# Performance work log

Measured on AMD Instinct MI355X. Metric: run time of the kernel, lower is better.

## Reference

```python
import jax, jax.numpy as jnp
import numpy as np

N = 50000
E = 600000
IN_DIM = 128
D = 32          # out_dim per head
H = 4           # heads
M = 3           # num metapaths
HID = 128       # semantic attention hidden
NEG_SLOPE = 0.2


def setup_inputs() -> dict:
    key = jax.random.key(0)
    ks = jax.random.split(key, 12)
    x = jax.random.normal(ks[0], (N, IN_DIM), dtype=jnp.float32)
    mp_edge_index = jax.random.randint(ks[1], (M, 2, E), 0, N, dtype=jnp.int64)
    s = 1.0 / np.sqrt(IN_DIM)
    W = jax.random.normal(ks[2], (M, IN_DIM, H * D), dtype=jnp.float32) * s
    att_src = jax.random.normal(ks[3], (M, H, D), dtype=jnp.float32) * (1.0 / np.sqrt(D))
    att_dst = jax.random.normal(ks[4], (M, H, D), dtype=jnp.float32) * (1.0 / np.sqrt(D))
    bias = jnp.zeros((M, H * D), dtype=jnp.float32)
    ln_gamma = jnp.ones((H * D,), dtype=jnp.float32)
    ln_beta = jnp.zeros((H * D,), dtype=jnp.float32)
    sem_W1 = jax.random.normal(ks[5], (H * D, HID), dtype=jnp.float32) * (1.0 / np.sqrt(H * D))
    sem_b1 = jnp.zeros((HID,), dtype=jnp.float32)
    sem_W2 = jax.random.normal(ks[6], (HID, 1), dtype=jnp.float32) * (1.0 / np.sqrt(HID))
    return dict(x=x, mp_edge_index=mp_edge_index, W=W, att_src=att_src,
                att_dst=att_dst, bias=bias, ln_gamma=ln_gamma, ln_beta=ln_beta,
                sem_W1=sem_W1, sem_b1=sem_b1, sem_W2=sem_W2)


def _gat_conv(x, edge_index, W_m, a_src, a_dst, b_m):
    # PyG GATConv (add_self_loops=True, concat=True). x: [N, F_in]
    n = x.shape[0]
    h = (x @ W_m).reshape(n, H, D)                       # [N, H, D]
    loops = jnp.arange(n, dtype=edge_index.dtype)
    src = jnp.concatenate([edge_index[0], loops])        # [E+N]
    dst = jnp.concatenate([edge_index[1], loops])
    alpha_s = jnp.einsum('nhd,hd->nh', h, a_src)         # [N, H]
    alpha_d = jnp.einsum('nhd,hd->nh', h, a_dst)
    e = jax.nn.leaky_relu(alpha_s[src] + alpha_d[dst], NEG_SLOPE)  # [E+N, H]
    # segment softmax over edges grouped by destination node
    e_max = jax.ops.segment_max(e, dst, num_segments=n)
    e = jnp.exp(e - e_max[dst])
    denom = jax.ops.segment_sum(e, dst, num_segments=n)
    alpha = e / (denom[dst] + 1e-16)                     # [E+N, H]
    msg = h[src] * alpha[:, :, None]                     # [E+N, H, D]
    out = jax.ops.segment_sum(msg, dst, num_segments=n)  # [N, H, D]
    return out.reshape(n, H * D) + b_m


def _layer_norm(y, gamma, beta):
    mu = y.mean(-1, keepdims=True)
    var = y.var(-1, keepdims=True)
    return (y - mu) * jax.lax.rsqrt(var + 1e-5) * gamma + beta


def reference(x, mp_edge_index, W, att_src, att_dst, bias, ln_gamma, ln_beta,
              sem_W1, sem_b1, sem_W2):
    embs = []
    for i in range(M):
        emb = _gat_conv(x, mp_edge_index[i], W[i], att_src[i], att_dst[i], bias[i])
        emb = jax.nn.elu(_layer_norm(emb, ln_gamma, ln_beta))
        embs.append(emb)
    z = jnp.stack(embs, axis=1)                          # [N, M, H*D]
    # semantic attention
    w = (jnp.tanh(z @ sem_W1 + sem_b1) @ sem_W2).mean(0)  # [M, 1]
    beta = jax.nn.softmax(w, axis=0)                      # [M, 1]
    out_emb = (beta[None, :, :] * z).sum(1)               # [N, H*D]
    att_mp = beta.squeeze()                               # [M]
    return out_emb, att_mp
```

## Files before the change

### kernel.cpp

```cpp
#include <hip/hip_runtime.h>
#include <hip/hip_bf16.h>

#define N_NODES 50000
#define N_EDGES 600000
#define NMETA   3
#define LTOT (NMETA * N_NODES)
#define SPAN_SHIFT 9
#define NBUCK 98
#define BCAP 8192
#define NCHUNK 147
#define NABLK 782
#define NSLOT (NMETA * NBUCK * BCAP)
#define NSEMBLK ((LTOT / 16 + 3) / 4)
#define LOG2E 1.4426950408889634f

typedef unsigned short u16;
typedef short bf16x8 __attribute__((ext_vector_type(8)));
typedef float f32x4 __attribute__((ext_vector_type(4)));

__device__ __forceinline__ float bf2f(u16 v) {
    union { unsigned int u; float f; } x; x.u = ((unsigned int)v) << 16; return x.f;
}
__device__ __forceinline__ float u2f(unsigned int u) {
    union { unsigned int u; float f; } x; x.u = u; return x.f;
}
__device__ __forceinline__ u16 f2bf(float f) {
    return __hip_bfloat16_raw(__float2bfloat16(f)).x;
}

#if __has_builtin(__builtin_amdgcn_fdot2_f32_bf16)
#define HAS_DOT2 1
typedef __bf16 bf16x2v __attribute__((ext_vector_type(2)));
__device__ __forceinline__ float dot2bf(unsigned hp, unsigned ep, float acc) {
    return __builtin_amdgcn_fdot2_f32_bf16(
        __builtin_bit_cast(bf16x2v, hp), __builtin_bit_cast(bf16x2v, ep), acc, false);
}
#else
#define HAS_DOT2 0
#endif

__global__ __launch_bounds__(256) void k_build1(
    const int* __restrict__ ei, int* __restrict__ gcnt,
    unsigned* __restrict__ pairs,
    const float* __restrict__ W, const float* __restrict__ W1,
    u16* __restrict__ WT, u16* __restrict__ W1T)
{
    const int bid = blockIdx.x;
    const int t = threadIdx.x;
    if (bid >= NMETA * NCHUNK) {
        int idx = (bid - NMETA * NCHUNK) * 256 + t;
        if (idx < NMETA * 16384) {
            int m = idx >> 14, r = idx & 16383;
            int col = r >> 7, k = r & 127;
            WT[idx] = f2bf(W[(m << 14) + k * 128 + col]);
        } else {
            int r = idx - NMETA * 16384;
            int col = r >> 7, k = r & 127;
            W1T[r] = f2bf(W1[k * 128 + col]);
        }
        return;
    }
    const int m = bid / NCHUNK;
    const int e0 = (bid % NCHUNK) * 4096;
    __shared__ int cnt[NBUCK];
    __shared__ int gbase[NBUCK];
    if (t < NBUCK) cnt[t] = 0;
    __syncthreads();
    const int* srcp = ei + (size_t)m * 2 * N_EDGES;
    const int* dstp = srcp + N_EDGES;
    int sa[16], da[16], sl[16];
    #pragma unroll
    for (int j = 0; j < 16; ++j) {
        int e = e0 + j * 256 + t;
        if (e < N_EDGES) {
            int s = srcp[e], d = dstp[e];
            if ((unsigned)s >= N_NODES) s = 0;
            if ((unsigned)d >= N_NODES) d = 0;
            sa[j] = s; da[j] = d;
            sl[j] = atomicAdd(&cnt[d >> SPAN_SHIFT], 1);
        } else sl[j] = -1;
    }
    __syncthreads();
    if (t < NBUCK) gbase[t] = atomicAdd(&gcnt[(m * NBUCK + t) * 16], cnt[t]);
    __syncthreads();
    #pragma unroll
    for (int j = 0; j < 16; ++j) {
        if (sl[j] < 0) continue;
        int b = da[j] >> SPAN_SHIFT;
        int pos = gbase[b] + sl[j];
        if (pos < BCAP)
            pairs[(size_t)(m * NBUCK + b) * BCAP + pos] =
                ((unsigned)(da[j] & 511) << 23) | (unsigned)(sa[j] * 128);
    }
}

__global__ __launch_bounds__(256) void k_build2(
    const int* __restrict__ gcnt, const unsigned* __restrict__ pairs,
    int* __restrict__ row_start, int* __restrict__ row_end, int* __restrict__ eidx,
    int* __restrict__ ptot,
    const float* __restrict__ x, const u16* __restrict__ WT,
    const float* __restrict__ att_src, const float* __restrict__ att_dst,
    u16* __restrict__ h, float* __restrict__ alpha_s, float* __restrict__ alpha_d)
{
    const int bid = blockIdx.x;
    const int t = threadIdx.x;
    if (bid < NMETA * NBUCK) {
        const int m = bid / NBUCK, b = bid % NBUCK;
        __shared__ int cnt[512];
        __shared__ int off[512];
        __shared__ int wsum[4];
        int nb = gcnt[(m * NBUCK + b) * 16]; if (nb > BCAP) nb = BCAP;
        const int base = (m * NBUCK + b) * BCAP;
        cnt[t] = 0; cnt[t + 256] = 0;
        __syncthreads();
        for (int e = t; e < nb; e += 256) {
            int dl = (int)(pairs[(size_t)base + e] >> 23);
            atomicAdd(&cnt[dl], 1);
        }
        __syncthreads();
        int c0 = cnt[2 * t], c1 = cnt[2 * t + 1];
        int v0p = (c0 + 3) & ~3, v1p = (c1 + 3) & ~3;
        int s = v0p + v1p;
        int lane = t & 63, wv = t >> 6;
        int incl = s;
        #pragma unroll
        for (int o = 1; o < 64; o <<= 1) {
            int u = __shfl_up(incl, o);
            if (lane >= o) incl += u;
        }
        if (lane == 63) wsum[wv] = incl;
        __syncthreads();
        int woff = 0;
        for (int i = 0; i < wv; ++i) woff += wsum[i];
        int ex = woff + incl - s;
        off[2 * t] = ex;
        off[2 * t + 1] = ex + v0p;
        if (t == 255) {
            int tot = ex + v0p + v1p;
            ptot[m * NBUCK + b] = tot < BCAP ? tot : BCAP;
        }
        for (int q = ex + c0; q < ex + v0p && q < BCAP; ++q) eidx[base + q] = 0;
        for (int q = ex + v0p + c1; q < ex + v0p + v1p && q < BCAP; ++q) eidx[base + q] = 0;
        __syncthreads();
        const int node0 = b << SPAN_SHIFT;
        for (int i = t; i < 512; i += 256) {
            int n = node0 + i;
            if (n < N_NODES) {
                int st = base + off[i];
                row_start[m * N_NODES + n] = st;
                row_end[m * N_NODES + n]   = st + cnt[i];
            }
        }
        __syncthreads();
        for (int e = t; e < nb; e += 256) {
            unsigned pv = pairs[(size_t)base + e];
            int dl = (int)(pv >> 23);
            int pos = atomicAdd(&off[dl], 1);
            if (pos >= BCAP) continue;
            eidx[base + pos] = (int)pv;
        }
        return;
    }
    const int g = bid - NMETA * NBUCK;
    const int bx = g % NABLK, m = g / NABLK;
    const int wv = t >> 6, lane = t & 63;
    const int row0 = (bx * 4 + wv) * 16;
    if (row0 >= N_NODES) return;
    const int lhi = lane >> 4, llo = lane & 15;
    const float* xrow = x + (size_t)(row0 + llo) * 128 + lhi * 8;
    bf16x8 a[4];
    #pragma unroll
    for (int ks = 0; ks < 4; ++ks) {
        float4 f0 = *(const float4*)(xrow + ks * 32);
        float4 f1 = *(const float4*)(xrow + ks * 32 + 4);
        bf16x8 av;
        av[0] = f2bf(f0.x); av[1] = f2bf(f0.y); av[2] = f2bf(f0.z); av[3] = f2bf(f0.w);
        av[4] = f2bf(f1.x); av[5] = f2bf(f1.y); av[6] = f2bf(f1.z); av[7] = f2bf(f1.w);
        a[ks] = av;
    }
    const u16* wbase = WT + (size_t)m * 16384 + (size_t)llo * 128 + lhi * 8;
    u16* hm = h + ((size_t)m * N_NODES + row0) * 128;
    float sp[4][4], dp[4][4];
    #pragma unroll
    for (int i = 0; i < 4; ++i)
        #pragma unroll
        for (int r = 0; r < 4; ++r) { sp[i][r] = 0.f; dp[i][r] = 0.f; }
    #pragma unroll
    for (int cf = 0; cf < 8; ++cf) {
        f32x4 acc = {0.f, 0.f, 0.f, 0.f};
        const u16* wp = wbase + cf * 16 * 128;
        #pragma unroll
        for (int ks = 0; ks < 4; ++ks) {
            bf16x8 bb = *(const bf16x8*)(wp + ks * 32);
            acc = __builtin_amdgcn_mfma_f32_16x16x32_bf16(a[ks], bb, acc, 0, 0, 0);
        }
        const int col = cf * 16 + llo;
        const int hh = cf >> 1;
        const float as = att_src[m * 128 + col];
        const float adv = att_dst[m * 128 + col];
        #pragma unroll
        for (int r = 0; r < 4; ++r) {
            hm[(size_t)(lhi * 4 + r) * 128 + col] = f2bf(acc[r]);
            sp[hh][r] += acc[r] * as;
            dp[hh][r] += acc[r] * adv;
        }
    }
    #pragma unroll
    for (int o = 1; o <= 8; o <<= 1) {
        #pragma unroll
        for (int i = 0; i < 4; ++i)
            #pragma unroll
            for (int r = 0; r < 4; ++r) {
                sp[i][r] += __shfl_xor(sp[i][r], o);
                dp[i][r] += __shfl_xor(dp[i][r], o);
            }
    }
    if (llo == 0) {
        #pragma unroll
        for (int r = 0; r < 4; ++r) {
            int n = row0 + lhi * 4 + r;
            f32x4 vs = {sp[0][r] * LOG2E, sp[1][r] * LOG2E, sp[2][r] * LOG2E, sp[3][r] * LOG2E};
            f32x4 vd = {dp[0][r] * LOG2E, dp[1][r] * LOG2E, dp[2][r] * LOG2E, dp[3][r] * LOG2E};
            *(f32x4*)(alpha_s + ((size_t)m * N_NODES + n) * 4) = vs;
            *(f32x4*)(alpha_d + ((size_t)m * N_NODES + n) * 4) = vd;
        }
    }
}

__global__ __launch_bounds__(256) void k_ew(
    const int* __restrict__ ptot, int* __restrict__ eidx,
    const float* __restrict__ alpha_s, const float* __restrict__ alpha_d,
    u16* __restrict__ ew)
{
    for (int sidx = blockIdx.x * 256 + threadIdx.x; sidx < NSLOT; sidx += gridDim.x * 256) {
        const int bucket = sidx >> 13;
        const int i = sidx & (BCAP - 1);
        if (i >= ptot[bucket]) continue;
        const int m = bucket / NBUCK, b = bucket % NBUCK;
        const int node0 = b << SPAN_SHIFT;
        int v = eidx[sidx];
        int src128 = v & 0x7FFFFF;
        int dl = (unsigned)v >> 23;
        const float* as_m = alpha_s + (size_t)m * N_NODES * 4;
        const float* ad_m = alpha_d + (size_t)m * N_NODES * 4;
        f32x4 as4 = *(const f32x4*)(as_m + (src128 >> 5));
        f32x4 ad4 = *(const f32x4*)(ad_m + (size_t)(node0 + dl) * 4);
        u16* ewp = ew + (size_t)(sidx >> 2) * 16 + (sidx & 3);
        #pragma unroll
        for (int k = 0; k < 4; ++k) {
            float pre = as4[k] + ad4[k];
            pre = fmaxf(pre, 0.2f * pre);
            ewp[k * 4] = f2bf(exp2f(pre));
        }
        eidx[sidx] = src128 * 2;
    }
}

__global__ __launch_bounds__(256) void k_gather(
    const int* __restrict__ row_start, const int* __restrict__ row_end,
    const int* __restrict__ eidx, const u16* __restrict__ ew,
    const float* __restrict__ alpha_s, const float* __restrict__ alpha_d,
    const u16* __restrict__ h,
    const float* __restrict__ bias, const float* __restrict__ gamma,
    const float* __restrict__ lbeta,
    u16* __restrict__ z)
{
    long long w = ((long long)blockIdx.x * blockDim.x + threadIdx.x) >> 6;
    if (w >= (long long)LTOT) return;
    int m = (int)(w / N_NODES), n = (int)(w % N_NODES);
    int lane = threadIdx.x & 63, hh = lane >> 4;
    const char* h_m = (const char*)(h + (size_t)m * N_NODES * 128);
    const char* ewb = (const char*)ew;
    const int lb = lane * 4;
    const float* as_m = alpha_s + (size_t)m * N_NODES * 4;
    const float* ad_m = alpha_d + (size_t)m * N_NODES * 4;
    float pre = as_m[n * 4 + hh] + ad_m[n * 4 + hh];
    pre = fmaxf(pre, 0.2f * pre);
    float ev = exp2f(pre);
    float esum = ev;
    unsigned hv = *(const unsigned*)(h_m + (size_t)n * 256 + lb);
    float acc0 = ev * u2f(hv << 16), acc1 = ev * u2f(hv & 0xffff0000u);
    int p = row_start[m * N_NODES + n];
    const int end = row_end[m * N_NODES + n];
    for (; p + 3 < end; p += 4) {
        int4 o4 = *(const int4*)(eidx + p);
        uint2 ewv = *(const uint2*)(ewb + (size_t)(p + hh) * 8);
        unsigned h1 = *(const unsigned*)(h_m + o4.x + lb);
        unsigned h2 = *(const unsigned*)(h_m + o4.y + lb);
        unsigned h3 = *(const unsigned*)(h_m + o4.z + lb);
        unsigned h4 = *(const unsigned*)(h_m + o4.w + lb);
#if HAS_DOT2
        unsigned lo12 = __builtin_amdgcn_perm(h2, h1, 0x05040100u);
        unsigned hi12 = __builtin_amdgcn_perm(h2, h1, 0x07060302u);
        unsigned lo34 = __builtin_amdgcn_perm(h4, h3, 0x05040100u);
        unsigned hi34 = __builtin_amdgcn_perm(h4, h3, 0x07060302u);
        acc0 = dot2bf(lo12, ewv.x, acc0);
        acc1 = dot2bf(hi12, ewv.x, acc1);
        acc0 = dot2bf(lo34, ewv.y, acc0);
        acc1 = dot2bf(hi34, ewv.y, acc1);
        esum = dot2bf(0x3F803F80u, ewv.x, esum);
        esum = dot2bf(0x3F803F80u, ewv.y, esum);
#else
        float e1 = u2f(ewv.x << 16), e2 = u2f(ewv.x & 0xffff0000u);
        float e3 = u2f(ewv.y << 16), e4 = u2f(ewv.y & 0xffff0000u);
        esum += (e1 + e2) + (e3 + e4);
        acc0 += e1 * u2f(h1 << 16) + e2 * u2f(h2 << 16)
              + e3 * u2f(h3 << 16) + e4 * u2f(h4 << 16);
        acc1 += e1 * u2f(h1 & 0xffff0000u) + e2 * u2f(h2 & 0xffff0000u)
              + e3 * u2f(h3 & 0xffff0000u) + e4 * u2f(h4 & 0xffff0000u);
#endif
    }
    for (; p < end; ++p) {
        int o1 = eidx[p];
        float e1 = bf2f(*(const u16*)(ewb + (size_t)((p & ~3) + hh) * 8 + (p & 3) * 2));
        unsigned h1 = *(const unsigned*)(h_m + o1 + lb);
        esum += e1;
        acc0 += e1 * u2f(h1 << 16);
        acc1 += e1 * u2f(h1 & 0xffff0000u);
    }
    float rinv = 1.f / (esum + 1e-16f);
    float v0 = acc0 * rinv + bias[m * 128 + lane * 2];
    float v1 = acc1 * rinv + bias[m * 128 + lane * 2 + 1];
    float s1 = v0 + v1, s2 = v0 * v0 + v1 * v1;
    #pragma unroll
    for (int o = 32; o >= 1; o >>= 1) { s1 += __shfl_xor(s1, o); s2 += __shfl_xor(s2, o); }
    float mu = s1 * (1.f / 128.f);
    float var = s2 * (1.f / 128.f) - mu * mu;
    float rs = rsqrtf(var + 1e-5f);
    float o0 = (v0 - mu) * rs * gamma[lane * 2]     + lbeta[lane * 2];
    float o1 = (v1 - mu) * rs * gamma[lane * 2 + 1] + lbeta[lane * 2 + 1];
    o0 = o0 > 0.f ? o0 : (__expf(o0) - 1.f);
    o1 = o1 > 0.f ? o1 : (__expf(o1) - 1.f);
    ushort2 outv; outv.x = f2bf(o0); outv.y = f2bf(o1);
    *(ushort2*)(z + ((size_t)n * NMETA + m) * 128 + lane * 2) = outv;
}

__global__ __launch_bounds__(256) void k_sem(
    const u16* __restrict__ z, const u16* __restrict__ W1T,
    const float* __restrict__ b1, const float* __restrict__ W2,
    float4* __restrict__ partial)
{
    __shared__ float part[NMETA];
    const int t = threadIdx.x;
    if (t < NMETA) part[t] = 0.f;
    __syncthreads();
    const int wv = t >> 6, lane = t & 63;
    const int row0 = (blockIdx.x * 4 + wv) * 16;
    if (row0 < LTOT) {
        const int lhi = lane >> 4, llo = lane & 15;
        const u16* zrow = z + (size_t)(row0 + llo) * 128 + lhi * 8;
        bf16x8 a[4];
        #pragma unroll
        for (int ks = 0; ks < 4; ++ks) a[ks] = *(const bf16x8*)(zrow + ks * 32);
        const u16* wb = W1T + (size_t)llo * 128 + lhi * 8;
        float rowacc[4] = {0.f, 0.f, 0.f, 0.f};
        #pragma unroll
        for (int cf = 0; cf < 8; ++cf) {
            f32x4 acc = {0.f, 0.f, 0.f, 0.f};
            const u16* wp = wb + cf * 16 * 128;
            #pragma unroll
            for (int ks = 0; ks < 4; ++ks) {
                bf16x8 bb = *(const bf16x8*)(wp + ks * 32);
                acc = __builtin_amdgcn_mfma_f32_16x16x32_bf16(a[ks], bb, acc, 0, 0, 0);
            }
            int col = cf * 16 + llo;
            float b1v = b1[col], w2v = W2[col];
            #pragma unroll
            for (int r = 0; r < 4; ++r) {
                float targ = acc[r] + b1v;
                float tv = 1.f - 2.f / (exp2f(targ * (2.f * LOG2E)) + 1.f);
                rowacc[r] += tv * w2v;
            }
        }
        #pragma unroll
        for (int o = 1; o <= 8; o <<= 1) {
            #pragma unroll
            for (int r = 0; r < 4; ++r) rowacc[r] += __shfl_xor(rowacc[r], o);
        }
        if (llo == 0) {
            #pragma unroll
            for (int r = 0; r < 4; ++r)
                atomicAdd(&part[(row0 + lhi * 4 + r) % NMETA], rowacc[r]);
        }
    }
    __syncthreads();
    if (t == 0)
        partial[blockIdx.x] = make_float4(part[0], part[1], part[2], 0.f);
}

__global__ __launch_bounds__(256) void k_beta(
    const float4* __restrict__ partial, float* __restrict__ betab,
    float* __restrict__ attout)
{
    const int t = threadIdx.x;
    float s0 = 0.f, s1 = 0.f, s2 = 0.f;
    for (int i = t; i < NSEMBLK; i += 256) {
        float4 v = partial[i];
        s0 += v.x; s1 += v.y; s2 += v.z;
    }
    #pragma unroll
    for (int o = 32; o >= 1; o >>= 1) {
        s0 += __shfl_xor(s0, o);
        s1 += __shfl_xor(s1, o);
        s2 += __shfl_xor(s2, o);
    }
    __shared__ float wsum[3][4];
    int lane = t & 63, wv = t >> 6;
    if (lane == 0) { wsum[0][wv] = s0; wsum[1][wv] = s1; wsum[2][wv] = s2; }
    __syncthreads();
    if (t == 0) {
        float w0 = (wsum[0][0] + wsum[0][1] + wsum[0][2] + wsum[0][3]) * (1.f / N_NODES);
        float w1 = (wsum[1][0] + wsum[1][1] + wsum[1][2] + wsum[1][3]) * (1.f / N_NODES);
        float w2 = (wsum[2][0] + wsum[2][1] + wsum[2][2] + wsum[2][3]) * (1.f / N_NODES);
        float mx = fmaxf(w0, fmaxf(w1, w2));
        float e0 = __expf(w0 - mx), e1 = __expf(w1 - mx), e2 = __expf(w2 - mx);
        float s = 1.f / (e0 + e1 + e2);
        float b0 = e0 * s, b1v = e1 * s, b2 = e2 * s;
        betab[0] = b0; betab[1] = b1v; betab[2] = b2;
        attout[0] = b0; attout[1] = b1v; attout[2] = b2;
    }
}

__global__ __launch_bounds__(256) void k_combine(
    const u16* __restrict__ z, const float* __restrict__ betab,
    float* __restrict__ out)
{
    int idx = blockIdx.x * blockDim.x + threadIdx.x;
    if (idx >= N_NODES * 16) return;
    int n = idx >> 4, c8 = (idx & 15) * 8;
    float b0 = betab[0], b1 = betab[1], b2 = betab[2];
    const u16* zp = z + (size_t)n * 384 + c8;
    uint4 a0 = *(const uint4*)(zp);
    uint4 a1 = *(const uint4*)(zp + 128);
    uint4 a2 = *(const uint4*)(zp + 256);
    const unsigned* p0 = (const unsigned*)&a0;
    const unsigned* p1 = (const unsigned*)&a1;
    const unsigned* p2 = (const unsigned*)&a2;
    float o[8];
    #pragma unroll
    for (int j = 0; j < 4; ++j) {
        o[2 * j]     = b0 * u2f(p0[j] << 16) + b1 * u2f(p1[j] << 16) + b2 * u2f(p2[j] << 16);
        o[2 * j + 1] = b0 * u2f(p0[j] & 0xffff0000u) + b1 * u2f(p1[j] & 0xffff0000u)
                     + b2 * u2f(p2[j] & 0xffff0000u);
    }
    float* op = out + (size_t)n * 128 + c8;
    *(float4*)(op)     = make_float4(o[0], o[1], o[2], o[3]);
    *(float4*)(op + 4) = make_float4(o[4], o[5], o[6], o[7]);
}

extern "C" void kernel_launch(void* const* d_in, const int* in_sizes, int n_in,
                              void* d_out, int out_size, void* d_ws, size_t ws_size,
                              hipStream_t stream) {
    const float* x       = (const float*)d_in[0];
    const int*   ei      = (const int*)d_in[1];
    const float* W       = (const float*)d_in[2];
    const float* att_src = (const float*)d_in[3];
    const float* att_dst = (const float*)d_in[4];
    const float* bias    = (const float*)d_in[5];
    const float* gamma   = (const float*)d_in[6];
    const float* lbeta   = (const float*)d_in[7];
    const float* W1      = (const float*)d_in[8];
    const float* b1      = (const float*)d_in[9];
    const float* W2      = (const float*)d_in[10];

    char* ws = (char*)d_ws;
    size_t off = 0;
    int* gcnt    = (int*)(ws + off);  off += sizeof(int) * 512 * 16;
    int* ptot    = (int*)(ws + off);  off += sizeof(int) * 512;
    float* betab = (float*)(ws + off); off += 64;
    const size_t zero_bytes = off;
    off = (off + 255) & ~(size_t)255;
    float4* partial = (float4*)(ws + off); off += sizeof(float4) * (NSEMBLK + 8);
    int* row_start = (int*)(ws + off); off += sizeof(int) * 150016;
    int* row_end   = (int*)(ws + off); off += sizeof(int) * 150016;
    u16* h      = (u16*)(ws + off);    off += sizeof(u16) * (size_t)NMETA * N_NODES * 128;
    float* alpha_s = (float*)(ws + off); off += sizeof(float) * (size_t)LTOT * 4;
    float* alpha_d = (float*)(ws + off); off += sizeof(float) * (size_t)LTOT * 4;
    u16* WT     = (u16*)(ws + off);    off += sizeof(u16) * (size_t)NMETA * 128 * 128;
    u16* W1T    = (u16*)(ws + off);    off += sizeof(u16) * (size_t)128 * 128;
    int* eidx   = (int*)(ws + off);    off += sizeof(int) * (size_t)NSLOT;
    u16* ew     = (u16*)(ws + off);    off += sizeof(u16) * (size_t)NSLOT * 4;
    unsigned* pairs = (unsigned*)(ws + off);
    u16* z = (u16*)(ws + off);
    off += sizeof(u16) * (size_t)N_NODES * NMETA * 128;
    if (ws_size < off) return;

    hipMemsetAsync(d_ws, 0, zero_bytes, stream);

    k_build1<<<dim3(NMETA * NCHUNK + 256), 256, 0, stream>>>(ei, gcnt, pairs, W, W1, WT, W1T);
    k_build2<<<dim3(NMETA * NBUCK + NABLK * NMETA), 256, 0, stream>>>(
        gcnt, pairs, row_start, row_end, eidx, ptot,
        x, WT, att_src, att_dst, h, alpha_s, alpha_d);
    k_ew<<<dim3(2048), 256, 0, stream>>>(ptot, eidx, alpha_s, alpha_d, ew);
    k_gather<<<dim3((LTOT + 3) / 4), 256, 0, stream>>>(row_start, row_end, eidx, ew,
                                                       alpha_s, alpha_d, h,
                                                       bias, gamma, lbeta, z);
    k_sem<<<dim3(NSEMBLK), 256, 0, stream>>>(z, W1T, b1, W2, partial);
    k_beta<<<1, 256, 0, stream>>>(partial, betab, (float*)d_out + (size_t)N_NODES * 128);
    k_combine<<<dim3((N_NODES * 16 + 255) / 256), 256, 0, stream>>>(z, betab, (float*)d_out);
}
```

Baseline: 262.8 us.

## Pre-convert x to bf16, drop eidx rewrite in k_ew, unroll gather by 8

Adds a bf16 conversion of x to the build1 kernel, so each of the three metapath projection passes reads half the bytes and skips per-element conversion. k_ew no longer writes back the remapped eidx. The gather instead masks and shifts the packed value at load time. The gather main loop is unrolled to 8 edges per iteration so more independent h loads are in flight. In exchange it adds an extra 12.8MB write of xb, placed in the pairs/z scratch region, and a little more ALU work per edge.

```diff
diff --git a/kernel.cpp b/kernel.cpp
--- a/kernel.cpp
+++ b/kernel.cpp
@@ -12,6 +12,7 @@
 #define NABLK 782
 #define NSLOT (NMETA * NBUCK * BCAP)
 #define NSEMBLK ((LTOT / 16 + 3) / 4)
+#define PREPX_BLKS 800
 #define LOG2E 1.4426950408889634f
 
 typedef unsigned short u16;
@@ -43,10 +44,21 @@
     const int* __restrict__ ei, int* __restrict__ gcnt,
     unsigned* __restrict__ pairs,
     const float* __restrict__ W, const float* __restrict__ W1,
-    u16* __restrict__ WT, u16* __restrict__ W1T)
+    u16* __restrict__ WT, u16* __restrict__ W1T,
+    const float* __restrict__ x, u16* __restrict__ xb)
 {
     const int bid = blockIdx.x;
     const int t = threadIdx.x;
+    if (bid >= NMETA * NCHUNK + 256) {
+        const int stride = PREPX_BLKS * 256;
+        for (int i = (bid - (NMETA * NCHUNK + 256)) * 256 + t; i < N_NODES * 32; i += stride) {
+            float4 v = ((const float4*)x)[i];
+            ushort4 o;
+            o.x = f2bf(v.x); o.y = f2bf(v.y); o.z = f2bf(v.z); o.w = f2bf(v.w);
+            ((ushort4*)xb)[i] = o;
+        }
+        return;
+    }
     if (bid >= NMETA * NCHUNK) {
         int idx = (bid - NMETA * NCHUNK) * 256 + t;
         if (idx < NMETA * 16384) {
@@ -98,7 +110,7 @@
     const int* __restrict__ gcnt, const unsigned* __restrict__ pairs,
     int* __restrict__ row_start, int* __restrict__ row_end, int* __restrict__ eidx,
     int* __restrict__ ptot,
-    const float* __restrict__ x, const u16* __restrict__ WT,
+    const u16* __restrict__ xb, const u16* __restrict__ WT,
     const float* __restrict__ att_src, const float* __restrict__ att_dst,
     u16* __restrict__ h, float* __restrict__ alpha_s, float* __restrict__ alpha_d)
 {
@@ -167,17 +179,10 @@
     const int row0 = (bx * 4 + wv) * 16;
     if (row0 >= N_NODES) return;
     const int lhi = lane >> 4, llo = lane & 15;
-    const float* xrow = x + (size_t)(row0 + llo) * 128 + lhi * 8;
+    const u16* xrow = xb + (size_t)(row0 + llo) * 128 + lhi * 8;
     bf16x8 a[4];
     #pragma unroll
-    for (int ks = 0; ks < 4; ++ks) {
-        float4 f0 = *(const float4*)(xrow + ks * 32);
-        float4 f1 = *(const float4*)(xrow + ks * 32 + 4);
-        bf16x8 av;
-        av[0] = f2bf(f0.x); av[1] = f2bf(f0.y); av[2] = f2bf(f0.z); av[3] = f2bf(f0.w);
-        av[4] = f2bf(f1.x); av[5] = f2bf(f1.y); av[6] = f2bf(f1.z); av[7] = f2bf(f1.w);
-        a[ks] = av;
-    }
+    for (int ks = 0; ks < 4; ++ks) a[ks] = *(const bf16x8*)(xrow + ks * 32);
     const u16* wbase = WT + (size_t)m * 16384 + (size_t)llo * 128 + lhi * 8;
     u16* hm = h + ((size_t)m * N_NODES + row0) * 128;
     float sp[4][4], dp[4][4];
@@ -228,7 +233,7 @@
 }
 
 __global__ __launch_bounds__(256) void k_ew(
-    const int* __restrict__ ptot, int* __restrict__ eidx,
+    const int* __restrict__ ptot, const int* __restrict__ eidx,
     const float* __restrict__ alpha_s, const float* __restrict__ alpha_d,
     u16* __restrict__ ew)
 {
@@ -252,7 +257,6 @@
             pre = fmaxf(pre, 0.2f * pre);
             ewp[k * 4] = f2bf(exp2f(pre));
         }
-        eidx[sidx] = src128 * 2;
     }
 }
 
@@ -282,13 +286,63 @@
     float acc0 = ev * u2f(hv << 16), acc1 = ev * u2f(hv & 0xffff0000u);
     int p = row_start[m * N_NODES + n];
     const int end = row_end[m * N_NODES + n];
+    for (; p + 7 < end; p += 8) {
+        int4 vA = *(const int4*)(eidx + p);
+        int4 vB = *(const int4*)(eidx + p + 4);
+        uint2 ewA = *(const uint2*)(ewb + (size_t)(p + hh) * 8);
+        uint2 ewB = *(const uint2*)(ewb + (size_t)(p + 4 + hh) * 8);
+        unsigned h1 = *(const unsigned*)(h_m + ((vA.x & 0x7FFFFF) << 1) + lb);
+        unsigned h2 = *(const unsigned*)(h_m + ((vA.y & 0x7FFFFF) << 1) + lb);
+        unsigned h3 = *(const unsigned*)(h_m + ((vA.z & 0x7FFFFF) << 1) + lb);
+        unsigned h4 = *(const unsigned*)(h_m + ((vA.w & 0x7FFFFF) << 1) + lb);
+        unsigned h5 = *(const unsigned*)(h_m + ((vB.x & 0x7FFFFF) << 1) + lb);
+        unsigned h6 = *(const unsigned*)(h_m + ((vB.y & 0x7FFFFF) << 1) + lb);
+        unsigned h7 = *(const unsigned*)(h_m + ((vB.z & 0x7FFFFF) << 1) + lb);
+        unsigned h8 = *(const unsigned*)(h_m + ((vB.w & 0x7FFFFF) << 1) + lb);
+#if HAS_DOT2
+        unsigned lo12 = __builtin_amdgcn_perm(h2, h1, 0x05040100u);
+        unsigned hi12 = __builtin_amdgcn_perm(h2, h1, 0x07060302u);
+        unsigned lo34 = __builtin_amdgcn_perm(h4, h3, 0x05040100u);
+        unsigned hi34 = __builtin_amdgcn_perm(h4, h3, 0x07060302u);
+        unsigned lo56 = __builtin_amdgcn_perm(h6, h5, 0x05040100u);
+        unsigned hi56 = __builtin_amdgcn_perm(h6, h5, 0x07060302u);
+        unsigned lo78 = __builtin_amdgcn_perm(h8, h7, 0x05040100u);
+        unsigned hi78 = __builtin_amdgcn_perm(h8, h7, 0x07060302u);
+        acc0 = dot2bf(lo12, ewA.x, acc0);
+        acc1 = dot2bf(hi12, ewA.x, acc1);
+        acc0 = dot2bf(lo34, ewA.y, acc0);
+        acc1 = dot2bf(hi34, ewA.y, acc1);
+        acc0 = dot2bf(lo56, ewB.x, acc0);
+        acc1 = dot2bf(hi56, ewB.x, acc1);
+        acc0 = dot2bf(lo78, ewB.y, acc0);
+        acc1 = dot2bf(hi78, ewB.y, acc1);
+        esum = dot2bf(0x3F803F80u, ewA.x, esum);
+        esum = dot2bf(0x3F803F80u, ewA.y, esum);
+        esum = dot2bf(0x3F803F80u, ewB.x, esum);
+        esum = dot2bf(0x3F803F80u, ewB.y, esum);
+#else
+        float e1 = u2f(ewA.x << 16), e2 = u2f(ewA.x & 0xffff0000u);
+        float e3 = u2f(ewA.y << 16), e4 = u2f(ewA.y & 0xffff0000u);
+        float e5 = u2f(ewB.x << 16), e6 = u2f(ewB.x & 0xffff0000u);
+        float e7 = u2f(ewB.y << 16), e8 = u2f(ewB.y & 0xffff0000u);
+        esum += ((e1 + e2) + (e3 + e4)) + ((e5 + e6) + (e7 + e8));
+        acc0 += e1 * u2f(h1 << 16) + e2 * u2f(h2 << 16)
+              + e3 * u2f(h3 << 16) + e4 * u2f(h4 << 16)
+              + e5 * u2f(h5 << 16) + e6 * u2f(h6 << 16)
+              + e7 * u2f(h7 << 16) + e8 * u2f(h8 << 16);
+        acc1 += e1 * u2f(h1 & 0xffff0000u) + e2 * u2f(h2 & 0xffff0000u)
+              + e3 * u2f(h3 & 0xffff0000u) + e4 * u2f(h4 & 0xffff0000u)
+              + e5 * u2f(h5 & 0xffff0000u) + e6 * u2f(h6 & 0xffff0000u)
+              + e7 * u2f(h7 & 0xffff0000u) + e8 * u2f(h8 & 0xffff0000u);
+#endif
+    }
     for (; p + 3 < end; p += 4) {
-        int4 o4 = *(const int4*)(eidx + p);
+        int4 vA = *(const int4*)(eidx + p);
         uint2 ewv = *(const uint2*)(ewb + (size_t)(p + hh) * 8);
-        unsigned h1 = *(const unsigned*)(h_m + o4.x + lb);
-        unsigned h2 = *(const unsigned*)(h_m + o4.y + lb);
-        unsigned h3 = *(const unsigned*)(h_m + o4.z + lb);
-        unsigned h4 = *(const unsigned*)(h_m + o4.w + lb);
+        unsigned h1 = *(const unsigned*)(h_m + ((vA.x & 0x7FFFFF) << 1) + lb);
+        unsigned h2 = *(const unsigned*)(h_m + ((vA.y & 0x7FFFFF) << 1) + lb);
+        unsigned h3 = *(const unsigned*)(h_m + ((vA.z & 0x7FFFFF) << 1) + lb);
+        unsigned h4 = *(const unsigned*)(h_m + ((vA.w & 0x7FFFFF) << 1) + lb);
 #if HAS_DOT2
         unsigned lo12 = __builtin_amdgcn_perm(h2, h1, 0x05040100u);
         unsigned hi12 = __builtin_amdgcn_perm(h2, h1, 0x07060302u);
@@ -311,9 +365,9 @@
 #endif
     }
     for (; p < end; ++p) {
-        int o1 = eidx[p];
+        int v = eidx[p];
         float e1 = bf2f(*(const u16*)(ewb + (size_t)((p & ~3) + hh) * 8 + (p & 3) * 2));
-        unsigned h1 = *(const unsigned*)(h_m + o1 + lb);
+        unsigned h1 = *(const unsigned*)(h_m + ((v & 0x7FFFFF) << 1) + lb);
         esum += e1;
         acc0 += e1 * u2f(h1 << 16);
         acc1 += e1 * u2f(h1 & 0xffff0000u);
@@ -481,16 +535,18 @@
     int* eidx   = (int*)(ws + off);    off += sizeof(int) * (size_t)NSLOT;
     u16* ew     = (u16*)(ws + off);    off += sizeof(u16) * (size_t)NSLOT * 4;
     unsigned* pairs = (unsigned*)(ws + off);
-    u16* z = (u16*)(ws + off);
+    u16* xb = (u16*)(ws + off + sizeof(unsigned) * (size_t)NSLOT);
+    u16* z  = (u16*)(ws + off);
     off += sizeof(u16) * (size_t)N_NODES * NMETA * 128;
     if (ws_size < off) return;
 
     hipMemsetAsync(d_ws, 0, zero_bytes, stream);
 
-    k_build1<<<dim3(NMETA * NCHUNK + 256), 256, 0, stream>>>(ei, gcnt, pairs, W, W1, WT, W1T);
+    k_build1<<<dim3(NMETA * NCHUNK + 256 + PREPX_BLKS), 256, 0, stream>>>(
+        ei, gcnt, pairs, W, W1, WT, W1T, x, xb);
     k_build2<<<dim3(NMETA * NBUCK + NABLK * NMETA), 256, 0, stream>>>(
         gcnt, pairs, row_start, row_end, eidx, ptot,
-        x, WT, att_src, att_dst, h, alpha_s, alpha_d);
+        xb, WT, att_src, att_dst, h, alpha_s, alpha_d);
     k_ew<<<dim3(2048), 256, 0, stream>>>(ptot, eidx, alpha_s, alpha_d, ew);
     k_gather<<<dim3((LTOT + 3) / 4), 256, 0, stream>>>(row_start, row_end, eidx, ew,
                                                        alpha_s, alpha_d, h,
```

After: 249.8 us. 4.9% less time.

## Pre-convert x to bf16, split gather wave into two edge halves

Applied to the files above, without the earlier changes.

A new group of blocks in the first build kernel converts x to bf16 once, so the three per-metapath projection passes read half the bytes and skip repeated conversion. The gather kernel now splits each wave into two 32-lane halves, each handling alternate edge pairs with 8-byte h loads, and merges them with a cross-half shuffle. Padding slots are tagged with a sentinel value so k_ew writes zero weights for them, and the remainder loop disappears. k_ew no longer rewrites eidx in place. This trades fewer, wider gather loads and no tail loop for padding work, extra shuffles and a layernorm reduction that spans both halves.

```diff
diff --git a/kernel.cpp b/kernel.cpp
--- a/kernel.cpp
+++ b/kernel.cpp
@@ -12,6 +12,7 @@
 #define NABLK 782
 #define NSLOT (NMETA * NBUCK * BCAP)
 #define NSEMBLK ((LTOT / 16 + 3) / 4)
+#define PREPX_BLKS 800
 #define LOG2E 1.4426950408889634f
 
 typedef unsigned short u16;
@@ -43,10 +44,21 @@
     const int* __restrict__ ei, int* __restrict__ gcnt,
     unsigned* __restrict__ pairs,
     const float* __restrict__ W, const float* __restrict__ W1,
-    u16* __restrict__ WT, u16* __restrict__ W1T)
+    u16* __restrict__ WT, u16* __restrict__ W1T,
+    const float* __restrict__ x, u16* __restrict__ xb)
 {
     const int bid = blockIdx.x;
     const int t = threadIdx.x;
+    if (bid >= NMETA * NCHUNK + 256) {
+        const int stride = PREPX_BLKS * 256;
+        for (int i = (bid - (NMETA * NCHUNK + 256)) * 256 + t; i < N_NODES * 32; i += stride) {
+            float4 v = ((const float4*)x)[i];
+            ushort4 o;
+            o.x = f2bf(v.x); o.y = f2bf(v.y); o.z = f2bf(v.z); o.w = f2bf(v.w);
+            ((ushort4*)xb)[i] = o;
+        }
+        return;
+    }
     if (bid >= NMETA * NCHUNK) {
         int idx = (bid - NMETA * NCHUNK) * 256 + t;
         if (idx < NMETA * 16384) {
@@ -98,7 +110,7 @@
     const int* __restrict__ gcnt, const unsigned* __restrict__ pairs,
     int* __restrict__ row_start, int* __restrict__ row_end, int* __restrict__ eidx,
     int* __restrict__ ptot,
-    const float* __restrict__ x, const u16* __restrict__ WT,
+    const u16* __restrict__ xb, const u16* __restrict__ WT,
     const float* __restrict__ att_src, const float* __restrict__ att_dst,
     u16* __restrict__ h, float* __restrict__ alpha_s, float* __restrict__ alpha_d)
 {
@@ -139,8 +151,8 @@
             int tot = ex + v0p + v1p;
             ptot[m * NBUCK + b] = tot < BCAP ? tot : BCAP;
         }
-        for (int q = ex + c0; q < ex + v0p && q < BCAP; ++q) eidx[base + q] = 0;
-        for (int q = ex + v0p + c1; q < ex + v0p + v1p && q < BCAP; ++q) eidx[base + q] = 0;
+        for (int q = ex + c0; q < ex + v0p && q < BCAP; ++q) eidx[base + q] = 64;
+        for (int q = ex + v0p + c1; q < ex + v0p + v1p && q < BCAP; ++q) eidx[base + q] = 64;
         __syncthreads();
         const int node0 = b << SPAN_SHIFT;
         for (int i = t; i < 512; i += 256) {
@@ -167,17 +179,10 @@
     const int row0 = (bx * 4 + wv) * 16;
     if (row0 >= N_NODES) return;
     const int lhi = lane >> 4, llo = lane & 15;
-    const float* xrow = x + (size_t)(row0 + llo) * 128 + lhi * 8;
+    const u16* xrow = xb + (size_t)(row0 + llo) * 128 + lhi * 8;
     bf16x8 a[4];
     #pragma unroll
-    for (int ks = 0; ks < 4; ++ks) {
-        float4 f0 = *(const float4*)(xrow + ks * 32);
-        float4 f1 = *(const float4*)(xrow + ks * 32 + 4);
-        bf16x8 av;
-        av[0] = f2bf(f0.x); av[1] = f2bf(f0.y); av[2] = f2bf(f0.z); av[3] = f2bf(f0.w);
-        av[4] = f2bf(f1.x); av[5] = f2bf(f1.y); av[6] = f2bf(f1.z); av[7] = f2bf(f1.w);
-        a[ks] = av;
-    }
+    for (int ks = 0; ks < 4; ++ks) a[ks] = *(const bf16x8*)(xrow + ks * 32);
     const u16* wbase = WT + (size_t)m * 16384 + (size_t)llo * 128 + lhi * 8;
     u16* hm = h + ((size_t)m * N_NODES + row0) * 128;
     float sp[4][4], dp[4][4];
@@ -228,7 +233,7 @@
 }
 
 __global__ __launch_bounds__(256) void k_ew(
-    const int* __restrict__ ptot, int* __restrict__ eidx,
+    const int* __restrict__ ptot, const int* __restrict__ eidx,
     const float* __restrict__ alpha_s, const float* __restrict__ alpha_d,
     u16* __restrict__ ew)
 {
@@ -236,23 +241,27 @@
         const int bucket = sidx >> 13;
         const int i = sidx & (BCAP - 1);
         if (i >= ptot[bucket]) continue;
+        int v = eidx[sidx];
+        u16* ewp = ew + (size_t)(sidx >> 2) * 16 + (sidx & 3);
+        if (v & 127) {
+            #pragma unroll
+            for (int k = 0; k < 4; ++k) ewp[k * 4] = 0;
+            continue;
+        }
         const int m = bucket / NBUCK, b = bucket % NBUCK;
         const int node0 = b << SPAN_SHIFT;
-        int v = eidx[sidx];
         int src128 = v & 0x7FFFFF;
         int dl = (unsigned)v >> 23;
         const float* as_m = alpha_s + (size_t)m * N_NODES * 4;
         const float* ad_m = alpha_d + (size_t)m * N_NODES * 4;
         f32x4 as4 = *(const f32x4*)(as_m + (src128 >> 5));
         f32x4 ad4 = *(const f32x4*)(ad_m + (size_t)(node0 + dl) * 4);
-        u16* ewp = ew + (size_t)(sidx >> 2) * 16 + (sidx & 3);
         #pragma unroll
         for (int k = 0; k < 4; ++k) {
             float pre = as4[k] + ad4[k];
             pre = fmaxf(pre, 0.2f * pre);
             ewp[k * 4] = f2bf(exp2f(pre));
         }
-        eidx[sidx] = src128 * 2;
     }
 }
 
@@ -268,71 +277,82 @@
     long long w = ((long long)blockIdx.x * blockDim.x + threadIdx.x) >> 6;
     if (w >= (long long)LTOT) return;
     int m = (int)(w / N_NODES), n = (int)(w % N_NODES);
-    int lane = threadIdx.x & 63, hh = lane >> 4;
+    int lane = threadIdx.x & 63;
+    const int il = lane & 31;
+    const int half = lane >> 5;
+    const int hd = il >> 3;
+    const int c0 = il * 4;
+    const int lboff = il * 8;
     const char* h_m = (const char*)(h + (size_t)m * N_NODES * 128);
     const char* ewb = (const char*)ew;
-    const int lb = lane * 4;
     const float* as_m = alpha_s + (size_t)m * N_NODES * 4;
     const float* ad_m = alpha_d + (size_t)m * N_NODES * 4;
-    float pre = as_m[n * 4 + hh] + ad_m[n * 4 + hh];
+    float pre = as_m[n * 4 + hd] + ad_m[n * 4 + hd];
     pre = fmaxf(pre, 0.2f * pre);
-    float ev = exp2f(pre);
+    float ev = (half == 0) ? exp2f(pre) : 0.f;
     float esum = ev;
-    unsigned hv = *(const unsigned*)(h_m + (size_t)n * 256 + lb);
-    float acc0 = ev * u2f(hv << 16), acc1 = ev * u2f(hv & 0xffff0000u);
-    int p = row_start[m * N_NODES + n];
-    const int end = row_end[m * N_NODES + n];
-    for (; p + 3 < end; p += 4) {
-        int4 o4 = *(const int4*)(eidx + p);
-        uint2 ewv = *(const uint2*)(ewb + (size_t)(p + hh) * 8);
-        unsigned h1 = *(const unsigned*)(h_m + o4.x + lb);
-        unsigned h2 = *(const unsigned*)(h_m + o4.y + lb);
-        unsigned h3 = *(const unsigned*)(h_m + o4.z + lb);
-        unsigned h4 = *(const unsigned*)(h_m + o4.w + lb);
+    uint2 hv = *(const uint2*)(h_m + (size_t)n * 256 + lboff);
+    float acc0 = ev * u2f(hv.x << 16);
+    float acc1 = ev * u2f(hv.x & 0xffff0000u);
+    float acc2 = ev * u2f(hv.y << 16);
+    float acc3 = ev * u2f(hv.y & 0xffff0000u);
+    int p = row_start[m * N_NODES + n] + half * 2;
+    const int pend = (row_end[m * N_NODES + n] + 3) & ~3;
+    for (; p < pend; p += 4) {
+        int2 v2 = *(const int2*)(eidx + p);
+        unsigned ewp = *(const unsigned*)(ewb + (size_t)(p >> 2) * 32 + hd * 8 + half * 4);
+        int offA = (v2.x & 0x7FFFFF) << 1;
+        int offB = (v2.y & 0x7FFFFF) << 1;
+        uint2 hA = *(const uint2*)(h_m + offA + lboff);
+        uint2 hB = *(const uint2*)(h_m + offB + lboff);
 #if HAS_DOT2
-        unsigned lo12 = __builtin_amdgcn_perm(h2, h1, 0x05040100u);
-        unsigned hi12 = __builtin_amdgcn_perm(h2, h1, 0x07060302u);
-        unsigned lo34 = __builtin_amdgcn_perm(h4, h3, 0x05040100u);
-        unsigned hi34 = __builtin_amdgcn_perm(h4, h3, 0x07060302u);
-        acc0 = dot2bf(lo12, ewv.x, acc0);
-        acc1 = dot2bf(hi12, ewv.x, acc1);
-        acc0 = dot2bf(lo34, ewv.y, acc0);
-        acc1 = dot2bf(hi34, ewv.y, acc1);
-        esum = dot2bf(0x3F803F80u, ewv.x, esum);
-        esum = dot2bf(0x3F803F80u, ewv.y, esum);
+        acc0 = dot2bf(__builtin_amdgcn_perm(hB.x, hA.x, 0x05040100u), ewp, acc0);
+        acc1 = dot2bf(__builtin_amdgcn_perm(hB.x, hA.x, 0x07060302u), ewp, acc1);
+        acc2 = dot2bf(__builtin_amdgcn_perm(hB.y, hA.y, 0x05040100u), ewp, acc2);
+        acc3 = dot2bf(__builtin_amdgcn_perm(hB.y, hA.y, 0x07060302u), ewp, acc3);
+        esum = dot2bf(0x3F803F80u, ewp, esum);
 #else
-        float e1 = u2f(ewv.x << 16), e2 = u2f(ewv.x & 0xffff0000u);
-        float e3 = u2f(ewv.y << 16), e4 = u2f(ewv.y & 0xffff0000u);
-        esum += (e1 + e2) + (e3 + e4);
-        acc0 += e1 * u2f(h1 << 16) + e2 * u2f(h2 << 16)
-              + e3 * u2f(h3 << 16) + e4 * u2f(h4 << 16);
-        acc1 += e1 * u2f(h1 & 0xffff0000u) + e2 * u2f(h2 & 0xffff0000u)
-              + e3 * u2f(h3 & 0xffff0000u) + e4 * u2f(h4 & 0xffff0000u);
+        float eA = u2f(ewp << 16), eB = u2f(ewp & 0xffff0000u);
+        esum += eA + eB;
+        acc0 += eA * u2f(hA.x << 16)        + eB * u2f(hB.x << 16);
+        acc1 += eA * u2f(hA.x & 0xffff0000u) + eB * u2f(hB.x & 0xffff0000u);
+        acc2 += eA * u2f(hA.y << 16)        + eB * u2f(hB.y << 16);
+        acc3 += eA * u2f(hA.y & 0xffff0000u) + eB * u2f(hB.y & 0xffff0000u);
 #endif
     }
-    for (; p < end; ++p) {
-        int o1 = eidx[p];
-        float e1 = bf2f(*(const u16*)(ewb + (size_t)((p & ~3) + hh) * 8 + (p & 3) * 2));
-        unsigned h1 = *(const unsigned*)(h_m + o1 + lb);
-        esum += e1;
-        acc0 += e1 * u2f(h1 << 16);
-        acc1 += e1 * u2f(h1 & 0xffff0000u);
-    }
+    acc0 += __shfl_xor(acc0, 32);
+    acc1 += __shfl_xor(acc1, 32);
+    acc2 += __shfl_xor(acc2, 32);
+    acc3 += __shfl_xor(acc3, 32);
+    esum += __shfl_xor(esum, 32);
     float rinv = 1.f / (esum + 1e-16f);
-    float v0 = acc0 * rinv + bias[m * 128 + lane * 2];
-    float v1 = acc1 * rinv + bias[m * 128 + lane * 2 + 1];
-    float s1 = v0 + v1, s2 = v0 * v0 + v1 * v1;
+    float4 bv = *(const float4*)(bias + m * 128 + c0);
+    float v0 = acc0 * rinv + bv.x;
+    float v1 = acc1 * rinv + bv.y;
+    float v2v = acc2 * rinv + bv.z;
+    float v3 = acc3 * rinv + bv.w;
+    float s1 = (v0 + v1) + (v2v + v3);
+    float s2 = (v0 * v0 + v1 * v1) + (v2v * v2v + v3 * v3);
     #pragma unroll
     for (int o = 32; o >= 1; o >>= 1) { s1 += __shfl_xor(s1, o); s2 += __shfl_xor(s2, o); }
-    float mu = s1 * (1.f / 128.f);
-    float var = s2 * (1.f / 128.f) - mu * mu;
+    float mu = s1 * (1.f / 256.f);
+    float var = s2 * (1.f / 256.f) - mu * mu;
     float rs = rsqrtf(var + 1e-5f);
-    float o0 = (v0 - mu) * rs * gamma[lane * 2]     + lbeta[lane * 2];
-    float o1 = (v1 - mu) * rs * gamma[lane * 2 + 1] + lbeta[lane * 2 + 1];
+    float4 gv = *(const float4*)(gamma + c0);
+    float4 lv = *(const float4*)(lbeta + c0);
+    float o0 = (v0 - mu) * rs * gv.x + lv.x;
+    float o1 = (v1 - mu) * rs * gv.y + lv.y;
+    float o2 = (v2v - mu) * rs * gv.z + lv.z;
+    float o3 = (v3 - mu) * rs * gv.w + lv.w;
     o0 = o0 > 0.f ? o0 : (__expf(o0) - 1.f);
     o1 = o1 > 0.f ? o1 : (__expf(o1) - 1.f);
-    ushort2 outv; outv.x = f2bf(o0); outv.y = f2bf(o1);
-    *(ushort2*)(z + ((size_t)n * NMETA + m) * 128 + lane * 2) = outv;
+    o2 = o2 > 0.f ? o2 : (__expf(o2) - 1.f);
+    o3 = o3 > 0.f ? o3 : (__expf(o3) - 1.f);
+    if (half == 0) {
+        ushort4 outv;
+        outv.x = f2bf(o0); outv.y = f2bf(o1); outv.z = f2bf(o2); outv.w = f2bf(o3);
+        *(ushort4*)(z + ((size_t)n * NMETA + m) * 128 + c0) = outv;
+    }
 }
 
 __global__ __launch_bounds__(256) void k_sem(
@@ -481,16 +501,18 @@
     int* eidx   = (int*)(ws + off);    off += sizeof(int) * (size_t)NSLOT;
     u16* ew     = (u16*)(ws + off);    off += sizeof(u16) * (size_t)NSLOT * 4;
     unsigned* pairs = (unsigned*)(ws + off);
-    u16* z = (u16*)(ws + off);
+    u16* xb = (u16*)(ws + off + sizeof(unsigned) * (size_t)NSLOT);
+    u16* z  = (u16*)(ws + off);
     off += sizeof(u16) * (size_t)N_NODES * NMETA * 128;
     if (ws_size < off) return;
 
     hipMemsetAsync(d_ws, 0, zero_bytes, stream);
 
-    k_build1<<<dim3(NMETA * NCHUNK + 256), 256, 0, stream>>>(ei, gcnt, pairs, W, W1, WT, W1T);
+    k_build1<<<dim3(NMETA * NCHUNK + 256 + PREPX_BLKS), 256, 0, stream>>>(
+        ei, gcnt, pairs, W, W1, WT, W1T, x, xb);
     k_build2<<<dim3(NMETA * NBUCK + NABLK * NMETA), 256, 0, stream>>>(
         gcnt, pairs, row_start, row_end, eidx, ptot,
-        x, WT, att_src, att_dst, h, alpha_s, alpha_d);
+        xb, WT, att_src, att_dst, h, alpha_s, alpha_d);
     k_ew<<<dim3(2048), 256, 0, stream>>>(ptot, eidx, alpha_s, alpha_d, ew);
     k_gather<<<dim3((LTOT + 3) / 4), 256, 0, stream>>>(row_start, row_end, eidx, ew,
                                                        alpha_s, alpha_d, h,
```

Measured after the change: 261.1 us. About the same (-0.7%).
